# Kernel optimization log

Hardware: AMD Instinct MI355X
Metric: run time of the kernel (lower is better)

The kernel has to match this reference:

```python
import jax, jax.numpy as jnp
import numpy as np

N = 1024   # nodes
F = 128    # raw feature dim (feat.shape[1])
D1 = 64    # dim1
D2 = 16    # dim2
ALPHA = 0.1
K1 = 2     # layer1 (APPNP steps)
K2 = 1     # layer2 (SpGEMM blocks)
E_HALF = 8192
P = 4096


def setup_inputs() -> dict:
    rng = np.random.default_rng(0)
    # symmetric, unique, loop-free edge set (required so that the original
    # transpose-coalesce step `x * sm` means value(u,v)*value(v,u))
    u = rng.integers(0, N, 20000)
    v = rng.integers(0, N, 20000)
    m = u != v
    u, v = u[m], v[m]
    lo, hi = np.minimum(u, v), np.maximum(u, v)
    pairs = np.unique(np.stack([lo, hi], 1), axis=0)[:E_HALF]  # [E_HALF, 2]
    ei = np.concatenate([pairs.T, pairs.T[::-1]], axis=1)      # [2, 2*E_HALF]
    ei = jnp.asarray(ei, dtype=jnp.int32)
    pos = jnp.asarray(rng.integers(0, N, (P, 2)), dtype=jnp.int32)

    key = jax.random.key(0)
    ks = jax.random.split(key, 10)
    s = 0.05
    return {
        "feat": jax.random.normal(ks[0], (N, F), jnp.float32),
        "W1": jax.random.normal(ks[1], (F, D1), jnp.float32) * s,
        "b1": jax.random.normal(ks[2], (D1,), jnp.float32) * s,
        "Wm1": jax.random.normal(ks[3], (2 * D1, D2), jnp.float32) * s,
        "bm1": jax.random.normal(ks[4], (D2,), jnp.float32) * s,
        "Wm2": jax.random.normal(ks[5], (2 * D1, D2), jnp.float32) * s,
        "bm2": jax.random.normal(ks[6], (D2,), jnp.float32) * s,
        "W3": jax.random.normal(ks[7], (D2 + 1, D2), jnp.float32) * s,
        "b3": jax.random.normal(ks[8], (D2,), jnp.float32) * s,
        "ei": ei,
        "pos": pos,
    }


def reference(feat, W1, b1, Wm1, bm1, Wm2, bm2, W3, b3, ei, pos):
    n = feat.shape[0]
    dt = feat.dtype

    # lin1 (dropouts/LN/ReLU disabled by default args)
    x = feat @ W1 + b1                                   # [n, D1]

    # APPNP with gcn norm + self loops: A_hat = D^-1/2 (A+I) D^-1/2
    A = jnp.zeros((n, n), dt).at[ei[0], ei[1]].add(1.0)
    A = A + jnp.eye(n, dtype=dt)
    dinv = 1.0 / jnp.sqrt(A.sum(1))
    Ahat = dinv[:, None] * A * dinv[None, :]
    h = x
    for _ in range(K1):
        x = (1.0 - ALPHA) * (Ahat @ x) + ALPHA * h

    xx = x[pos[:, 0]] * x[pos[:, 1]]                     # [P, D1]

    val = jnp.concatenate([x[ei[0]], x[ei[1]]], 1)       # [E, 2*D1]
    xe = val @ Wm1 + bm1                                 # [E, D2]
    mul = val @ Wm2 + bm2                                # [E, D2]

    # dense embedding of the sparse edge tensors (pattern = Se)
    Se = jnp.zeros((n, n), bool).at[ei[0], ei[1]].set(True)
    Sef = Se.astype(dt)
    Xd = jnp.zeros((n, n, D2), dt).at[ei[0], ei[1]].set(xe)
    Md = jnp.zeros((n, n, D2), dt).at[ei[0], ei[1]].set(mul)
    Scur = Sef

    for _ in range(K2):
        # per-feature SpGEMM: result[:,:,m] = X[:,:,m] @ M[:,:,m]
        prod = jnp.einsum('uvm,vwm->uwm', Xd, Md)        # [n, n, D2]
        Snew = (Scur @ Sef) > 0                          # structural nnz of product
        U = Snew | Se                                    # merged edge set (sparse_cat)
        # value = [scattered product values, indicator of edge_index membership]
        value = jnp.concatenate([prod, Sef[..., None]], -1)   # [n, n, D2+1]
        # mlps_3 applied only on merged edges; implicit zero elsewhere
        Xd = jnp.where(U[..., None], value @ W3 + b3, jnp.zeros((), dt))
        Scur = U.astype(dt)

    # transpose-coalesce trick: value(u,v) * value(v,u) (U is symmetric)
    xs = Xd * jnp.transpose(Xd, (1, 0, 2))
    ef = xs[pos[:, 0], pos[:, 1]]                        # [P, D2] (zero off-pattern)
    out = (ef.sum(-1) + xx.sum(-1))[:, None]             # [P, 1]
    return out
```

## Files before the change

kernel.cpp:

```cpp
#include <hip/hip_runtime.h>

#define NN   1024
#define FD   128
#define DD1  64
#define DD2  16
#define DSTRIDE 64
#define AC   0.1f

__device__ unsigned int       g_Tv[NN * NN];
__device__ int                g_deg[NN];
__device__ int                g_cnt[NN];
__device__ float              g_dinv[NN];
__device__ unsigned long long g_bits[NN * 16];
__device__ int                g_adj[NN * DSTRIDE];
__device__ float              g_x0[NN * DD1];
__device__ float              g_x1[NN * DD1];
__device__ float              g_x2[NN * DD1];
__device__ float              g_proj[NN * 64];
__device__ unsigned int       g_epoch;

__global__ void k1_gemm_scatter(const float* __restrict__ feat,
                                const float* __restrict__ W1,
                                const float* __restrict__ b1,
                                const int* __restrict__ ei0,
                                const int* __restrict__ ei1, int M) {
    __shared__ float s_f[4][FD];
    int tix = threadIdx.x;
    int tid = blockIdx.x * 256 + tix;
    unsigned int tag = g_epoch + 1u;
    if (tid < M) {
        int a = ei0[tid], b = ei1[tid];
        g_Tv[a * NN + b] = tag;
        atomicAdd(&g_deg[a], 1);
    }
    int wib = tix >> 6, lane = tix & 63;
    int n = blockIdx.x * 4 + wib;
    if (lane < 32)
        ((float4*)s_f[wib])[lane] = ((const float4*)(feat + n * FD))[lane];
    __syncthreads();
    const float* sf = s_f[wib];
    float acc = b1[lane];
    #pragma unroll 8
    for (int k = 0; k < FD; ++k) acc += sf[k] * W1[k * DD1 + lane];
    g_x0[n * DD1 + lane] = acc;
}

__global__ void k2_compact_prop1() {
    __shared__ int s_v[DSTRIDE];
    int u = blockIdx.x;
    int lane = threadIdx.x;
    unsigned int tag = g_epoch + 1u;
    const unsigned int* row = g_Tv + u * NN;
    int base = u * DSTRIDE;
    unsigned long long mymask = 0;
    int cnt = 0;
    #pragma unroll
    for (int i = 0; i < 16; ++i) {
        bool hit = (row[i * 64 + lane] == tag);
        unsigned long long mk = __ballot(hit);
        if (lane == i) mymask = mk;
        if (hit) {
            int p = __popcll(mk & ((1ULL << lane) - 1ULL));
            g_adj[base + cnt + p] = i * 64 + lane;
            s_v[cnt + p] = i * 64 + lane;
        }
        cnt += __popcll(mk);
    }
    if (lane < 16) g_bits[u * 16 + lane] = mymask;
    float du = rsqrtf((float)(cnt + 1));
    if (lane == 0) { g_cnt[u] = cnt; g_dinv[u] = du; }
    __syncthreads();
    float x0u = g_x0[u * DD1 + lane];
    float acc = 0.f;
    int j = 0;
    for (; j + 4 <= cnt; j += 4) {
        int v0 = s_v[j], v1 = s_v[j + 1], v2 = s_v[j + 2], v3 = s_v[j + 3];
        float a0 = g_x0[v0 * DD1 + lane], a1 = g_x0[v1 * DD1 + lane];
        float a2 = g_x0[v2 * DD1 + lane], a3 = g_x0[v3 * DD1 + lane];
        float d0 = rsqrtf((float)(g_deg[v0] + 1));
        float d1 = rsqrtf((float)(g_deg[v1] + 1));
        float d2 = rsqrtf((float)(g_deg[v2] + 1));
        float d3 = rsqrtf((float)(g_deg[v3] + 1));
        acc += d0 * a0 + d1 * a1 + d2 * a2 + d3 * a3;
    }
    for (; j < cnt; ++j) {
        int v = s_v[j];
        acc += rsqrtf((float)(g_deg[v] + 1)) * g_x0[v * DD1 + lane];
    }
    float ah = du * (acc + du * x0u);
    g_x1[u * DD1 + lane] = (1.0f - AC) * ah + AC * x0u;
}

__global__ void k3_prop2_proj(const float* __restrict__ Wm1,
                              const float* __restrict__ Wm2) {
    __shared__ float s_x2[DD1];
    int u = blockIdx.x;
    int lane = threadIdx.x;
    int cnt = g_cnt[u];
    int base = u * DSTRIDE;
    float acc = 0.f;
    int j = 0;
    for (; j + 4 <= cnt; j += 4) {
        int4 vv = *(const int4*)&g_adj[base + j];
        float a0 = g_x1[vv.x * DD1 + lane], a1 = g_x1[vv.y * DD1 + lane];
        float a2 = g_x1[vv.z * DD1 + lane], a3 = g_x1[vv.w * DD1 + lane];
        float d0 = g_dinv[vv.x], d1 = g_dinv[vv.y];
        float d2 = g_dinv[vv.z], d3 = g_dinv[vv.w];
        acc += d0 * a0 + d1 * a1 + d2 * a2 + d3 * a3;
    }
    for (; j < cnt; ++j) {
        int v = g_adj[base + j];
        acc += g_dinv[v] * g_x1[v * DD1 + lane];
    }
    float du = g_dinv[u];
    float x1u = g_x1[u * DD1 + lane];
    float ah = du * (acc + du * x1u);
    float x2v = (1.0f - AC) * ah + AC * g_x0[u * DD1 + lane];
    g_x2[u * DD1 + lane] = x2v;
    s_x2[lane] = x2v;
    __syncthreads();

    int g = lane >> 4, m = lane & 15;
    const float* Wp = ((g < 2) ? Wm1 : Wm2) + ((g & 1) ? DD1 * DD2 : 0);
    float s = 0.f;
    #pragma unroll 8
    for (int d = 0; d < DD1; ++d) s += s_x2[d] * Wp[d * DD2 + m];
    g_proj[u * 64 + lane] = s;
}

__global__ void k4_pair(const int* __restrict__ pos,
                        const float* __restrict__ bm1, const float* __restrict__ bm2,
                        const float* __restrict__ W3,  const float* __restrict__ b3,
                        float* __restrict__ out, int P) {
    __shared__ int s_ev[4][DSTRIDE];
    int tix  = threadIdx.x;
    int lane = tix & 63;
    int wib  = tix >> 6;
    int p    = (blockIdx.x * 256 + tix) >> 6;
    int grp  = lane >> 4;
    int m    = lane & 15;

    int u = pos[2 * p], wn = pos[2 * p + 1];
    const float* xu = g_x2 + u  * DD1;
    const float* xw = g_x2 + wn * DD1;

    float xx = xu[lane] * xw[lane];
    #pragma unroll
    for (int o = 32; o; o >>= 1) xx += __shfl_xor(xx, o);

    int cnt  = g_cnt[u];
    int base = u * DSTRIDE;
    int chunk = wn >> 6, bit = wn & 63;
    bool hit = false;
    int v = 0;
    if (lane < cnt) {
        v = g_adj[base + lane];
        hit = (g_bits[v * 16 + chunk] >> bit) & 1ULL;
    }
    unsigned long long mk = __ballot(hit);
    int nev = __popcll(mk);
    if (hit) {
        int rank = __popcll(mk & ((1ULL << lane) - 1ULL));
        s_ev[wib][rank] = v;
    }
    __syncthreads();

    bool s_uw = (g_bits[u * 16 + chunk] >> bit) & 1ULL;
    float res = xx;
    if (nev || s_uw) {
        float a1u = g_proj[u  * 64      + m];
        float b2u = g_proj[u  * 64 + 48 + m];
        float a1w = g_proj[wn * 64      + m];
        float b2w = g_proj[wn * 64 + 48 + m];
        float c1 = bm1[m], c2 = bm2[m];

        float p0 = 0.f, p1 = 0.f;
        for (int q0 = 0; q0 < nev; q0 += 4) {
            int q = q0 + grp;
            if (q < nev) {
                int vk = s_ev[wib][q];
                float b1v = g_proj[vk * 64 + 16 + m];
                float a2v = g_proj[vk * 64 + 32 + m];
                p0 += (c1 + a1u + b1v) * (c2 + a2v + b2w);
                p1 += (c1 + a1w + b1v) * (c2 + a2v + b2u);
            }
        }
        p0 += __shfl_xor(p0, 16); p0 += __shfl_xor(p0, 32);
        p1 += __shfl_xor(p1, 16); p1 += __shfl_xor(p1, 32);

        float se = s_uw ? 1.0f : 0.0f;
        float b3m = b3[m] + se * W3[16 * DD2 + m];
        float y0 = b3m, y1 = b3m;
        #pragma unroll
        for (int k = 0; k < DD2; ++k) {
            float wk  = W3[k * DD2 + m];
            y0 += __shfl(p0, k) * wk;
            y1 += __shfl(p1, k) * wk;
        }
        float ef = y0 * y1;
        #pragma unroll
        for (int o = 8; o; o >>= 1) ef += __shfl_xor(ef, o);
        res += ef;
    }
    if (lane == 0) out[p] = res;

    if (blockIdx.x == 0) {
        ((int4*)g_deg)[tix] = make_int4(0, 0, 0, 0);
        if (tix == 0) g_epoch = g_epoch + 1u;
    }
}

extern "C" void kernel_launch(void* const* d_in, const int* in_sizes, int n_in,
                              void* d_out, int out_size, void* d_ws, size_t ws_size,
                              hipStream_t stream) {
    const float* feat = (const float*)d_in[0];
    const float* W1   = (const float*)d_in[1];
    const float* b1   = (const float*)d_in[2];
    const float* Wm1  = (const float*)d_in[3];
    const float* bm1  = (const float*)d_in[4];
    const float* Wm2  = (const float*)d_in[5];
    const float* bm2  = (const float*)d_in[6];
    const float* W3   = (const float*)d_in[7];
    const float* b3   = (const float*)d_in[8];
    const int*   ei   = (const int*)d_in[9];
    const int*   pos  = (const int*)d_in[10];
    float* out = (float*)d_out;

    int M = in_sizes[9] / 2;
    int P = in_sizes[10] / 2;
    const int* ei0 = ei;
    const int* ei1 = ei + M;

    k1_gemm_scatter<<<256, 256, 0, stream>>>(feat, W1, b1, ei0, ei1, M);
    k2_compact_prop1<<<NN, 64, 0, stream>>>();
    k3_prop2_proj<<<NN, 64, 0, stream>>>(Wm1, Wm2);
    k4_pair<<<(P * 64 + 255) / 256, 256, 0, stream>>>(pos, bm1, bm2, W3, b3, out, P);
}
```

Baseline: 44.73 us.

## Build adjacency lists via atomic slots and warp bitonic sort instead of dense tag matrix

Drops the 1024x1024 epoch-tagged dense matrix. Edges are now appended directly into per-node adjacency slots with atomicAdd, then each row is sorted with a wave-level bitonic sort to get a deterministic order and build the bitmask. This removes the 4MB dense row scan in the compaction kernel. It also packs four nodes per 256-thread block and replaces shared-memory staging with shuffles. It assumes degree never exceeds 64, and any duplicate edges would now be stored twice instead of collapsing.

```diff
diff --git a/kernel.cpp b/kernel.cpp
--- a/kernel.cpp
+++ b/kernel.cpp
@@ -7,7 +7,6 @@
 #define DSTRIDE 64
 #define AC   0.1f
 
-__device__ unsigned int       g_Tv[NN * NN];
 __device__ int                g_deg[NN];
 __device__ int                g_cnt[NN];
 __device__ float              g_dinv[NN];
@@ -17,7 +16,6 @@
 __device__ float              g_x1[NN * DD1];
 __device__ float              g_x2[NN * DD1];
 __device__ float              g_proj[NN * 64];
-__device__ unsigned int       g_epoch;
 
 __global__ void k1_gemm_scatter(const float* __restrict__ feat,
                                 const float* __restrict__ W1,
@@ -27,11 +25,10 @@
     __shared__ float s_f[4][FD];
     int tix = threadIdx.x;
     int tid = blockIdx.x * 256 + tix;
-    unsigned int tag = g_epoch + 1u;
     if (tid < M) {
         int a = ei0[tid], b = ei1[tid];
-        g_Tv[a * NN + b] = tag;
-        atomicAdd(&g_deg[a], 1);
+        int slot = atomicAdd(&g_deg[a], 1);
+        g_adj[a * DSTRIDE + slot] = b;
     }
     int wib = tix >> 6, lane = tix & 63;
     int n = blockIdx.x * 4 + wib;
@@ -45,86 +42,86 @@
     g_x0[n * DD1 + lane] = acc;
 }
 
-__global__ void k2_compact_prop1() {
-    __shared__ int s_v[DSTRIDE];
-    int u = blockIdx.x;
-    int lane = threadIdx.x;
-    unsigned int tag = g_epoch + 1u;
-    const unsigned int* row = g_Tv + u * NN;
-    int base = u * DSTRIDE;
-    unsigned long long mymask = 0;
-    int cnt = 0;
+__global__ void k2_sort_prop1() {
+    __shared__ unsigned long long s_bm[4][16];
+    int tix = threadIdx.x;
+    int wib = tix >> 6, lane = tix & 63;
+    int u = blockIdx.x * 4 + wib;
+    int cnt = g_deg[u];
+
+    int v = (lane < cnt) ? g_adj[u * DSTRIDE + lane] : 0x7FFFFFFF;
     #pragma unroll
-    for (int i = 0; i < 16; ++i) {
-        bool hit = (row[i * 64 + lane] == tag);
-        unsigned long long mk = __ballot(hit);
-        if (lane == i) mymask = mk;
-        if (hit) {
-            int p = __popcll(mk & ((1ULL << lane) - 1ULL));
-            g_adj[base + cnt + p] = i * 64 + lane;
-            s_v[cnt + p] = i * 64 + lane;
+    for (int k = 2; k <= 64; k <<= 1) {
+        #pragma unroll
+        for (int j = k >> 1; j > 0; j >>= 1) {
+            int o = __shfl_xor(v, j);
+            bool up    = (lane & k) == 0;
+            bool upper = (lane & j) != 0;
+            int mn = min(v, o), mx = max(v, o);
+            v = (up == upper) ? mx : mn;
         }
-        cnt += __popcll(mk);
-    }
-    if (lane < 16) g_bits[u * 16 + lane] = mymask;
+    }
+    if (lane < cnt) g_adj[u * DSTRIDE + lane] = v;
+
+    if (lane < 16) s_bm[wib][lane] = 0ULL;
+    __syncthreads();
+    if (lane < cnt)
+        atomicOr(&s_bm[wib][v >> 6], 1ULL << (v & 63));
+    __syncthreads();
+    if (lane < 16) g_bits[u * 16 + lane] = s_bm[wib][lane];
+
     float du = rsqrtf((float)(cnt + 1));
     if (lane == 0) { g_cnt[u] = cnt; g_dinv[u] = du; }
-    __syncthreads();
+
+    float dv = (lane < cnt) ? rsqrtf((float)(g_deg[v] + 1)) : 0.f;
     float x0u = g_x0[u * DD1 + lane];
     float acc = 0.f;
     int j = 0;
     for (; j + 4 <= cnt; j += 4) {
-        int v0 = s_v[j], v1 = s_v[j + 1], v2 = s_v[j + 2], v3 = s_v[j + 3];
-        float a0 = g_x0[v0 * DD1 + lane], a1 = g_x0[v1 * DD1 + lane];
-        float a2 = g_x0[v2 * DD1 + lane], a3 = g_x0[v3 * DD1 + lane];
-        float d0 = rsqrtf((float)(g_deg[v0] + 1));
-        float d1 = rsqrtf((float)(g_deg[v1] + 1));
-        float d2 = rsqrtf((float)(g_deg[v2] + 1));
-        float d3 = rsqrtf((float)(g_deg[v3] + 1));
-        acc += d0 * a0 + d1 * a1 + d2 * a2 + d3 * a3;
-    }
-    for (; j < cnt; ++j) {
-        int v = s_v[j];
-        acc += rsqrtf((float)(g_deg[v] + 1)) * g_x0[v * DD1 + lane];
-    }
+        int   v0 = __shfl(v, j),     v1 = __shfl(v, j + 1);
+        int   v2 = __shfl(v, j + 2), v3 = __shfl(v, j + 3);
+        float d0 = __shfl(dv, j),     d1 = __shfl(dv, j + 1);
+        float d2 = __shfl(dv, j + 2), d3 = __shfl(dv, j + 3);
+        acc += d0 * g_x0[v0 * DD1 + lane] + d1 * g_x0[v1 * DD1 + lane]
+             + d2 * g_x0[v2 * DD1 + lane] + d3 * g_x0[v3 * DD1 + lane];
+    }
+    for (; j < cnt; ++j)
+        acc += __shfl(dv, j) * g_x0[__shfl(v, j) * DD1 + lane];
     float ah = du * (acc + du * x0u);
     g_x1[u * DD1 + lane] = (1.0f - AC) * ah + AC * x0u;
 }
 
 __global__ void k3_prop2_proj(const float* __restrict__ Wm1,
                               const float* __restrict__ Wm2) {
-    __shared__ float s_x2[DD1];
-    int u = blockIdx.x;
-    int lane = threadIdx.x;
+    int tix = threadIdx.x;
+    int wib = tix >> 6, lane = tix & 63;
+    int u = blockIdx.x * 4 + wib;
     int cnt = g_cnt[u];
-    int base = u * DSTRIDE;
+    int vl = (lane < cnt) ? g_adj[u * DSTRIDE + lane] : 0;
+    float dl = (lane < cnt) ? g_dinv[vl] : 0.f;
     float acc = 0.f;
     int j = 0;
     for (; j + 4 <= cnt; j += 4) {
-        int4 vv = *(const int4*)&g_adj[base + j];
-        float a0 = g_x1[vv.x * DD1 + lane], a1 = g_x1[vv.y * DD1 + lane];
-        float a2 = g_x1[vv.z * DD1 + lane], a3 = g_x1[vv.w * DD1 + lane];
-        float d0 = g_dinv[vv.x], d1 = g_dinv[vv.y];
-        float d2 = g_dinv[vv.z], d3 = g_dinv[vv.w];
-        acc += d0 * a0 + d1 * a1 + d2 * a2 + d3 * a3;
-    }
-    for (; j < cnt; ++j) {
-        int v = g_adj[base + j];
-        acc += g_dinv[v] * g_x1[v * DD1 + lane];
-    }
+        int   v0 = __shfl(vl, j),     v1 = __shfl(vl, j + 1);
+        int   v2 = __shfl(vl, j + 2), v3 = __shfl(vl, j + 3);
+        float d0 = __shfl(dl, j),     d1 = __shfl(dl, j + 1);
+        float d2 = __shfl(dl, j + 2), d3 = __shfl(dl, j + 3);
+        acc += d0 * g_x1[v0 * DD1 + lane] + d1 * g_x1[v1 * DD1 + lane]
+             + d2 * g_x1[v2 * DD1 + lane] + d3 * g_x1[v3 * DD1 + lane];
+    }
+    for (; j < cnt; ++j)
+        acc += __shfl(dl, j) * g_x1[__shfl(vl, j) * DD1 + lane];
     float du = g_dinv[u];
     float x1u = g_x1[u * DD1 + lane];
     float ah = du * (acc + du * x1u);
     float x2v = (1.0f - AC) * ah + AC * g_x0[u * DD1 + lane];
     g_x2[u * DD1 + lane] = x2v;
-    s_x2[lane] = x2v;
-    __syncthreads();
 
     int g = lane >> 4, m = lane & 15;
     const float* Wp = ((g < 2) ? Wm1 : Wm2) + ((g & 1) ? DD1 * DD2 : 0);
     float s = 0.f;
     #pragma unroll 8
-    for (int d = 0; d < DD1; ++d) s += s_x2[d] * Wp[d * DD2 + m];
+    for (int d = 0; d < DD1; ++d) s += __shfl(x2v, d) * Wp[d * DD2 + m];
     g_proj[u * 64 + lane] = s;
 }
 
@@ -204,10 +201,8 @@
     }
     if (lane == 0) out[p] = res;
 
-    if (blockIdx.x == 0) {
+    if (blockIdx.x == 0)
         ((int4*)g_deg)[tix] = make_int4(0, 0, 0, 0);
-        if (tix == 0) g_epoch = g_epoch + 1u;
-    }
 }
 
 extern "C" void kernel_launch(void* const* d_in, const int* in_sizes, int n_in,
@@ -232,7 +227,7 @@
     const int* ei1 = ei + M;
 
     k1_gemm_scatter<<<256, 256, 0, stream>>>(feat, W1, b1, ei0, ei1, M);
-    k2_compact_prop1<<<NN, 64, 0, stream>>>();
-    k3_prop2_proj<<<NN, 64, 0, stream>>>(Wm1, Wm2);
+    k2_sort_prop1<<<256, 256, 0, stream>>>();
+    k3_prop2_proj<<<256, 256, 0, stream>>>(Wm1, Wm2);
     k4_pair<<<(P * 64 + 255) / 256, 256, 0, stream>>>(pos, bm1, bm2, W3, b3, out, P);
 }
```

After: 42.76 us. 1.05x faster.
